# Kernel tuning notes

Hardware: AMD Instinct MI355X
Metric: run time of the kernel (lower is better)

The kernel has to match this reference:

```python
import jax, jax.numpy as jnp
import numpy as np

ORDER = 16
FRAME = 160
EPS = 1e-8


def setup_inputs() -> dict:
    key = jax.random.key(0)
    B, T = 64, 320000  # 64 utterances x 20s @ 16kHz; T % FRAME == 0
    x = jax.random.normal(key, (B, T), dtype=jnp.float32)
    return {"x": x}


def _lpc_residual(x):
    # x: [B, T] -> residual [B, T, 1]
    B, T = x.shape
    F = T // FRAME
    frm = x.reshape(B, F, FRAME)  # [B, F, 160]

    # Autocorrelation lags 0..ORDER (equiv. np.correlate(frm, frm, 'full')[160-1 : 160+16])
    r = jnp.stack(
        [jnp.sum(frm[..., : FRAME - k] * frm[..., k:], axis=-1) for k in range(ORDER + 1)],
        axis=-1,
    )  # [B, F, 17]

    # Levinson-Durbin recursion, batched over (B, F); loop over fixed small ORDER.
    a = jnp.zeros((B, F, ORDER + 1), dtype=x.dtype).at[..., 0].set(1.0)
    e = jnp.where(r[..., 0] != 0, r[..., 0], EPS)
    for i in range(1, ORDER + 1):
        # acc = r[i] - sum_{j=1}^{i-1} a[j] * r[i-j]
        acc = r[..., i] - jnp.sum(a[..., 1:i] * r[..., 1:i][..., ::-1], axis=-1)
        safe_e = jnp.where(e != 0, e, 1.0)
        k = jnp.where(e != 0, acc / safe_e, 0.0)
        a_new = a[..., 1:i] - k[..., None] * a[..., i - 1:0:-1]
        a = a.at[..., 1:i].set(a_new)
        a = a.at[..., i].set(k)
        e = jnp.maximum(e * (1.0 - k * k), EPS)

    # FIR filter: lfilter(a, [1.0], frm) -> res[n] = sum_k a[k] * frm[n-k] (zero-padded)
    res = a[..., 0:1] * frm
    for k in range(1, ORDER + 1):
        shifted = jnp.pad(frm, ((0, 0), (0, 0), (k, 0)))[..., :FRAME]
        res = res + a[..., k:k + 1] * shifted

    return res.reshape(B, T)[..., None]


def reference(x):
    return _lpc_residual(x)
```

## Files before the change

kernel.cpp:

```cpp
#include <hip/hip_runtime.h>

#define FRAME 160
#define ORDER 16
#define LPC_EPS 1e-8f
#define NF 32
#define BS 256
#define SEG 20
#define SX 164
#define AB 20
#define QPB (NF * FRAME / 4 / BS)

__global__ __launch_bounds__(BS, 4) void lpc_fused(const float* __restrict__ x,
                                                   float* __restrict__ out) {
    __shared__ float xs[NF * SX];
    __shared__ float rbuf[NF * AB];
    __shared__ float abuf[NF * AB];

    const int t = threadIdx.x;
    const long long base = (long long)blockIdx.x * (NF * FRAME);

#pragma unroll
    for (int it = 0; it < QPB; ++it) {
        int p = it * BS + t;
        int f = p / 40;
        int off = (p - f * 40) * 4;
        float4 v = *(const float4*)(x + base + 4 * p);
        *(float4*)(&xs[f * SX + off]) = v;
    }
    __syncthreads();

    const int fi = t >> 3;
    const int part = t & 7;
    const int sbase = SEG * part;

    float w[SEG + ORDER];
#pragma unroll
    for (int m = 0; m < (SEG + ORDER) / 4; ++m) {
        int idx = sbase + 4 * m;
        float4 v = make_float4(0.f, 0.f, 0.f, 0.f);
        if (idx < FRAME) v = *(const float4*)(&xs[fi * SX + idx]);
        w[4 * m + 0] = v.x; w[4 * m + 1] = v.y;
        w[4 * m + 2] = v.z; w[4 * m + 3] = v.w;
    }

    float pre[ORDER];
#pragma unroll
    for (int m = 0; m < ORDER / 4; ++m) {
        int idx = sbase - ORDER + 4 * m;
        float4 v = make_float4(0.f, 0.f, 0.f, 0.f);
        if (idx >= 0) v = *(const float4*)(&xs[fi * SX + idx]);
        pre[4 * m + 0] = v.x; pre[4 * m + 1] = v.y;
        pre[4 * m + 2] = v.z; pre[4 * m + 3] = v.w;
    }

    float r[ORDER + 1];
#pragma unroll
    for (int k = 0; k <= ORDER; ++k) r[k] = 0.f;
#pragma unroll
    for (int n = 0; n < SEG; ++n) {
#pragma unroll
        for (int k = 0; k <= ORDER; ++k) {
            r[k] = fmaf(w[n], w[n + k], r[k]);
        }
    }
#pragma unroll
    for (int k = 0; k <= ORDER; ++k) {
        r[k] += __shfl_xor(r[k], 1);
        r[k] += __shfl_xor(r[k], 2);
        r[k] += __shfl_xor(r[k], 4);
    }

    if (part == 0) {
#pragma unroll
        for (int m = 0; m < 4; ++m)
            *(float4*)(&rbuf[fi * AB + 4 * m]) =
                make_float4(r[4 * m], r[4 * m + 1], r[4 * m + 2], r[4 * m + 3]);
        rbuf[fi * AB + 16] = r[16];
    }
    __syncthreads();

    if (t < NF) {
        float rr[ORDER + 1];
#pragma unroll
        for (int m = 0; m < 4; ++m) {
            float4 v = *(const float4*)(&rbuf[t * AB + 4 * m]);
            rr[4 * m + 0] = v.x; rr[4 * m + 1] = v.y;
            rr[4 * m + 2] = v.z; rr[4 * m + 3] = v.w;
        }
        rr[16] = rbuf[t * AB + 16];

        float a[ORDER + 1];
        a[0] = 1.f;
#pragma unroll
        for (int j = 1; j <= ORDER; ++j) a[j] = 0.f;
        float e = (rr[0] != 0.f) ? rr[0] : LPC_EPS;
#pragma unroll
        for (int i = 1; i <= ORDER; ++i) {
            float acc = rr[i];
#pragma unroll
            for (int j = 1; j < i; ++j) acc -= a[j] * rr[i - j];
            float k = acc * __builtin_amdgcn_rcpf(e);
#pragma unroll
            for (int j = 1; 2 * j < i; ++j) {
                float aj = a[j], aij = a[i - j];
                a[j]     = aj  - k * aij;
                a[i - j] = aij - k * aj;
            }
            if ((i & 1) == 0) {
                int m = i >> 1;
                a[m] = a[m] - k * a[m];
            }
            a[i] = k;
            e = fmaxf(e * (1.f - k * k), LPC_EPS);
        }
#pragma unroll
        for (int m = 0; m < 4; ++m)
            *(float4*)(&abuf[t * AB + 4 * m]) =
                make_float4(a[4 * m + 1], a[4 * m + 2], a[4 * m + 3], a[4 * m + 4]);
    }
    __syncthreads();

    float a[ORDER + 1];
    a[0] = 1.f;
#pragma unroll
    for (int m = 0; m < 4; ++m) {
        float4 v = *(const float4*)(&abuf[fi * AB + 4 * m]);
        a[4 * m + 1] = v.x; a[4 * m + 2] = v.y;
        a[4 * m + 3] = v.z; a[4 * m + 4] = v.w;
    }

#pragma unroll
    for (int m = 0; m < SEG / 4; ++m) {
        float o[4];
#pragma unroll
        for (int i = 0; i < 4; ++i) {
            int n = 4 * m + i;
            float s = 0.f;
#pragma unroll
            for (int k = 0; k <= ORDER; ++k) {
                int j = n - k;
                float xv = (j >= 0) ? w[j] : pre[ORDER + j];
                s = fmaf(a[k], xv, s);
            }
            o[i] = s;
        }
        *(float4*)(&xs[fi * SX + sbase + 4 * m]) = make_float4(o[0], o[1], o[2], o[3]);
    }
    __syncthreads();

#pragma unroll
    for (int it = 0; it < QPB; ++it) {
        int p = it * BS + t;
        int f = p / 40;
        int off = (p - f * 40) * 4;
        float4 v = *(const float4*)(&xs[f * SX + off]);
        *(float4*)(out + base + 4 * p) = v;
    }
}

extern "C" void kernel_launch(void* const* d_in, const int* in_sizes, int n_in,
                              void* d_out, int out_size, void* d_ws, size_t ws_size,
                              hipStream_t stream) {
    const float* x = (const float*)d_in[0];
    float* out = (float*)d_out;
    int total = in_sizes[0];
    int n_frames = total / FRAME;
    int n_blocks = n_frames / NF;
    lpc_fused<<<n_blocks, BS, 0, stream>>>(x, out);
}
```

Measured before the change: 39.75 us.

## Process two tiles per block with register prefetch of the next tile

Each block now handles two consecutive 32-frame tiles. It loads the next tile's input into registers while computing autocorrelation, Levinson-Durbin and FIR for the current tile, so global load latency overlaps compute. The grid shrinks by half. This adds register pressure from the prefetch buffer and an extra barrier between tiles, and fewer blocks may reduce latency hiding across the device.

```diff
diff --git a/kernel.cpp b/kernel.cpp
--- a/kernel.cpp
+++ b/kernel.cpp
@@ -9,6 +9,8 @@
 #define SX 164
 #define AB 20
 #define QPB (NF * FRAME / 4 / BS)
+#define TILE (NF * FRAME)
+#define T 2
 
 __global__ __launch_bounds__(BS, 4) void lpc_fused(const float* __restrict__ x,
                                                    float* __restrict__ out) {
@@ -17,144 +19,166 @@
     __shared__ float abuf[NF * AB];
 
     const int t = threadIdx.x;
-    const long long base = (long long)blockIdx.x * (NF * FRAME);
-
-#pragma unroll
-    for (int it = 0; it < QPB; ++it) {
-        int p = it * BS + t;
-        int f = p / 40;
-        int off = (p - f * 40) * 4;
-        float4 v = *(const float4*)(x + base + 4 * p);
-        *(float4*)(&xs[f * SX + off]) = v;
-    }
-    __syncthreads();
-
     const int fi = t >> 3;
     const int part = t & 7;
     const int sbase = SEG * part;
 
-    float w[SEG + ORDER];
+    const long long tile0 = (long long)blockIdx.x * T;
+
+    float4 pf[QPB];
 #pragma unroll
-    for (int m = 0; m < (SEG + ORDER) / 4; ++m) {
-        int idx = sbase + 4 * m;
-        float4 v = make_float4(0.f, 0.f, 0.f, 0.f);
-        if (idx < FRAME) v = *(const float4*)(&xs[fi * SX + idx]);
-        w[4 * m + 0] = v.x; w[4 * m + 1] = v.y;
-        w[4 * m + 2] = v.z; w[4 * m + 3] = v.w;
+    for (int it = 0; it < QPB; ++it) {
+        int p = it * BS + t;
+        pf[it] = *(const float4*)(x + tile0 * TILE + 4 * p);
     }
 
-    float pre[ORDER];
 #pragma unroll
-    for (int m = 0; m < ORDER / 4; ++m) {
-        int idx = sbase - ORDER + 4 * m;
-        float4 v = make_float4(0.f, 0.f, 0.f, 0.f);
-        if (idx >= 0) v = *(const float4*)(&xs[fi * SX + idx]);
-        pre[4 * m + 0] = v.x; pre[4 * m + 1] = v.y;
-        pre[4 * m + 2] = v.z; pre[4 * m + 3] = v.w;
-    }
+    for (int tt = 0; tt < T; ++tt) {
+        const long long base = (tile0 + tt) * TILE;
 
-    float r[ORDER + 1];
 #pragma unroll
-    for (int k = 0; k <= ORDER; ++k) r[k] = 0.f;
+        for (int it = 0; it < QPB; ++it) {
+            int p = it * BS + t;
+            int f = p / 40;
+            int off = (p - f * 40) * 4;
+            *(float4*)(&xs[f * SX + off]) = pf[it];
+        }
+        __syncthreads();
+
+        if (tt + 1 < T) {
 #pragma unroll
-    for (int n = 0; n < SEG; ++n) {
+            for (int it = 0; it < QPB; ++it) {
+                int p = it * BS + t;
+                pf[it] = *(const float4*)(x + base + TILE + 4 * p);
+            }
+        }
+
+        float w[SEG + ORDER];
+#pragma unroll
+        for (int m = 0; m < (SEG + ORDER) / 4; ++m) {
+            int idx = sbase + 4 * m;
+            float4 v = make_float4(0.f, 0.f, 0.f, 0.f);
+            if (idx < FRAME) v = *(const float4*)(&xs[fi * SX + idx]);
+            w[4 * m + 0] = v.x; w[4 * m + 1] = v.y;
+            w[4 * m + 2] = v.z; w[4 * m + 3] = v.w;
+        }
+
+        float pre[ORDER];
+#pragma unroll
+        for (int m = 0; m < ORDER / 4; ++m) {
+            int idx = sbase - ORDER + 4 * m;
+            float4 v = make_float4(0.f, 0.f, 0.f, 0.f);
+            if (idx >= 0) v = *(const float4*)(&xs[fi * SX + idx]);
+            pre[4 * m + 0] = v.x; pre[4 * m + 1] = v.y;
+            pre[4 * m + 2] = v.z; pre[4 * m + 3] = v.w;
+        }
+
+        float r[ORDER + 1];
+#pragma unroll
+        for (int k = 0; k <= ORDER; ++k) r[k] = 0.f;
+#pragma unroll
+        for (int n = 0; n < SEG; ++n) {
+#pragma unroll
+            for (int k = 0; k <= ORDER; ++k) {
+                r[k] = fmaf(w[n], w[n + k], r[k]);
+            }
+        }
 #pragma unroll
         for (int k = 0; k <= ORDER; ++k) {
-            r[k] = fmaf(w[n], w[n + k], r[k]);
+            r[k] += __shfl_xor(r[k], 1);
+            r[k] += __shfl_xor(r[k], 2);
+            r[k] += __shfl_xor(r[k], 4);
         }
-    }
+
+        if (part == 0) {
 #pragma unroll
-    for (int k = 0; k <= ORDER; ++k) {
-        r[k] += __shfl_xor(r[k], 1);
-        r[k] += __shfl_xor(r[k], 2);
-        r[k] += __shfl_xor(r[k], 4);
-    }
+            for (int m = 0; m < 4; ++m)
+                *(float4*)(&rbuf[fi * AB + 4 * m]) =
+                    make_float4(r[4 * m], r[4 * m + 1], r[4 * m + 2], r[4 * m + 3]);
+            rbuf[fi * AB + 16] = r[16];
+        }
+        __syncthreads();
 
-    if (part == 0) {
+        if (t < NF) {
+            float rr[ORDER + 1];
 #pragma unroll
-        for (int m = 0; m < 4; ++m)
-            *(float4*)(&rbuf[fi * AB + 4 * m]) =
-                make_float4(r[4 * m], r[4 * m + 1], r[4 * m + 2], r[4 * m + 3]);
-        rbuf[fi * AB + 16] = r[16];
-    }
-    __syncthreads();
+            for (int m = 0; m < 4; ++m) {
+                float4 v = *(const float4*)(&rbuf[t * AB + 4 * m]);
+                rr[4 * m + 0] = v.x; rr[4 * m + 1] = v.y;
+                rr[4 * m + 2] = v.z; rr[4 * m + 3] = v.w;
+            }
+            rr[16] = rbuf[t * AB + 16];
 
-    if (t < NF) {
-        float rr[ORDER + 1];
+            float a[ORDER + 1];
+            a[0] = 1.f;
 #pragma unroll
-        for (int m = 0; m < 4; ++m) {
-            float4 v = *(const float4*)(&rbuf[t * AB + 4 * m]);
-            rr[4 * m + 0] = v.x; rr[4 * m + 1] = v.y;
-            rr[4 * m + 2] = v.z; rr[4 * m + 3] = v.w;
+            for (int j = 1; j <= ORDER; ++j) a[j] = 0.f;
+            float e = (rr[0] != 0.f) ? rr[0] : LPC_EPS;
+#pragma unroll
+            for (int i = 1; i <= ORDER; ++i) {
+                float acc = rr[i];
+#pragma unroll
+                for (int j = 1; j < i; ++j) acc -= a[j] * rr[i - j];
+                float k = acc * __builtin_amdgcn_rcpf(e);
+#pragma unroll
+                for (int j = 1; 2 * j < i; ++j) {
+                    float aj = a[j], aij = a[i - j];
+                    a[j]     = aj  - k * aij;
+                    a[i - j] = aij - k * aj;
+                }
+                if ((i & 1) == 0) {
+                    int m = i >> 1;
+                    a[m] = a[m] - k * a[m];
+                }
+                a[i] = k;
+                e = fmaxf(e * (1.f - k * k), LPC_EPS);
+            }
+#pragma unroll
+            for (int m = 0; m < 4; ++m)
+                *(float4*)(&abuf[t * AB + 4 * m]) =
+                    make_float4(a[4 * m + 1], a[4 * m + 2], a[4 * m + 3], a[4 * m + 4]);
         }
-        rr[16] = rbuf[t * AB + 16];
+        __syncthreads();
 
         float a[ORDER + 1];
         a[0] = 1.f;
 #pragma unroll
-        for (int j = 1; j <= ORDER; ++j) a[j] = 0.f;
-        float e = (rr[0] != 0.f) ? rr[0] : LPC_EPS;
-#pragma unroll
-        for (int i = 1; i <= ORDER; ++i) {
-            float acc = rr[i];
-#pragma unroll
-            for (int j = 1; j < i; ++j) acc -= a[j] * rr[i - j];
-            float k = acc * __builtin_amdgcn_rcpf(e);
-#pragma unroll
-            for (int j = 1; 2 * j < i; ++j) {
-                float aj = a[j], aij = a[i - j];
-                a[j]     = aj  - k * aij;
-                a[i - j] = aij - k * aj;
-            }
-            if ((i & 1) == 0) {
-                int m = i >> 1;
-                a[m] = a[m] - k * a[m];
-            }
-            a[i] = k;
-            e = fmaxf(e * (1.f - k * k), LPC_EPS);
+        for (int m = 0; m < 4; ++m) {
+            float4 v = *(const float4*)(&abuf[fi * AB + 4 * m]);
+            a[4 * m + 1] = v.x; a[4 * m + 2] = v.y;
+            a[4 * m + 3] = v.z; a[4 * m + 4] = v.w;
         }
-#pragma unroll
-        for (int m = 0; m < 4; ++m)
-            *(float4*)(&abuf[t * AB + 4 * m]) =
-                make_float4(a[4 * m + 1], a[4 * m + 2], a[4 * m + 3], a[4 * m + 4]);
-    }
-    __syncthreads();
-
-    float a[ORDER + 1];
-    a[0] = 1.f;
-#pragma unroll
-    for (int m = 0; m < 4; ++m) {
-        float4 v = *(const float4*)(&abuf[fi * AB + 4 * m]);
-        a[4 * m + 1] = v.x; a[4 * m + 2] = v.y;
-        a[4 * m + 3] = v.z; a[4 * m + 4] = v.w;
-    }
 
 #pragma unroll
-    for (int m = 0; m < SEG / 4; ++m) {
-        float o[4];
+        for (int m = 0; m < SEG / 4; ++m) {
+            float o[4];
 #pragma unroll
-        for (int i = 0; i < 4; ++i) {
-            int n = 4 * m + i;
-            float s = 0.f;
+            for (int i = 0; i < 4; ++i) {
+                int n = 4 * m + i;
+                float s = 0.f;
 #pragma unroll
-            for (int k = 0; k <= ORDER; ++k) {
-                int j = n - k;
-                float xv = (j >= 0) ? w[j] : pre[ORDER + j];
-                s = fmaf(a[k], xv, s);
+                for (int k = 0; k <= ORDER; ++k) {
+                    int j = n - k;
+                    float xv = (j >= 0) ? w[j] : pre[ORDER + j];
+                    s = fmaf(a[k], xv, s);
+                }
+                o[i] = s;
             }
-            o[i] = s;
+            *(float4*)(&xs[fi * SX + sbase + 4 * m]) =
+                make_float4(o[0], o[1], o[2], o[3]);
         }
-        *(float4*)(&xs[fi * SX + sbase + 4 * m]) = make_float4(o[0], o[1], o[2], o[3]);
-    }
-    __syncthreads();
+        __syncthreads();
 
 #pragma unroll
-    for (int it = 0; it < QPB; ++it) {
-        int p = it * BS + t;
-        int f = p / 40;
-        int off = (p - f * 40) * 4;
-        float4 v = *(const float4*)(&xs[f * SX + off]);
-        *(float4*)(out + base + 4 * p) = v;
+        for (int it = 0; it < QPB; ++it) {
+            int p = it * BS + t;
+            int f = p / 40;
+            int off = (p - f * 40) * 4;
+            float4 v = *(const float4*)(&xs[f * SX + off]);
+            *(float4*)(out + base + 4 * p) = v;
+        }
+
+        if (tt + 1 < T) __syncthreads();
     }
 }
 
@@ -165,6 +189,6 @@
     float* out = (float*)d_out;
     int total = in_sizes[0];
     int n_frames = total / FRAME;
-    int n_blocks = n_frames / NF;
+    int n_blocks = n_frames / NF / T;
     lpc_fused<<<n_blocks, BS, 0, stream>>>(x, out);
 }
```

Result: slower. 52.89 us (+33.1%).
